# Kernel tuning notes

Measured on AMD Instinct MI355X. Metric: run time of the kernel, lower is better.

## Reference

```python
import jax, jax.numpy as jnp
import numpy as np

THETA = 10000.0

def _rope(x, cos, sin):
    # x: [B, S, D]; cos/sin: [S, D/2]. Pairs are (x[..., 2i], x[..., 2i+1]) treated as complex.
    xr = x.reshape(*x.shape[:-1], -1, 2)
    x0, x1 = xr[..., 0], xr[..., 1]
    o0 = x0 * cos - x1 * sin
    o1 = x0 * sin + x1 * cos
    return jnp.stack([o0, o1], axis=-1).reshape(x.shape)

def setup_inputs() -> dict:
    key = jax.random.key(0)
    ks = jax.random.split(key, 7)
    B, S, D = 4, 2048, 1024
    sd = 1.0 / np.sqrt(D)
    return {
        "x": jax.random.normal(ks[0], (B, S, D), dtype=jnp.float32),
        "wq_w": jax.random.normal(ks[1], (D, D), dtype=jnp.float32) * sd,
        "wq_b": jax.random.normal(ks[2], (D,), dtype=jnp.float32) * 0.01,
        "wk_w": jax.random.normal(ks[3], (D, D), dtype=jnp.float32) * sd,
        "wk_b": jax.random.normal(ks[4], (D,), dtype=jnp.float32) * 0.01,
        "wv_w": jax.random.normal(ks[5], (D, D), dtype=jnp.float32) * sd,
        "wv_b": jax.random.normal(ks[6], (D,), dtype=jnp.float32) * 0.01,
    }

def reference(x, wq_w, wq_b, wk_w, wk_b, wv_w, wv_b):
    B, S, D = x.shape
    # QKV projections (torch Linear: y = x @ W.T + b)
    q = jnp.einsum('bsd,ed->bse', x, wq_w) + wq_b
    k = jnp.einsum('bsd,ed->bse', x, wk_w) + wk_b
    v = jnp.einsum('bsd,ed->bse', x, wv_w) + wv_b
    # Rotary embedding: freqs_cis[t, i] = exp(i * t / theta^(2i/D))
    inv_freq = 1.0 / (THETA ** (jnp.arange(0, D, 2, dtype=jnp.float32) / D))  # [D/2]
    ang = jnp.arange(S, dtype=jnp.float32)[:, None] * inv_freq[None, :]  # [S, D/2]
    cos, sin = jnp.cos(ang), jnp.sin(ang)
    q = _rope(q, cos, sin)
    k = _rope(k, cos, sin)
    # Full (non-causal, single-head) attention with scale 1/sqrt(dim)
    scores = jnp.einsum('bqd,bkd->bqk', q, k) / jnp.sqrt(jnp.float32(D))
    probs = jax.nn.softmax(scores.astype(jnp.float32), axis=-1)
    return jnp.einsum('bqk,bkd->bqd', probs, v)
```

## Files before the change

### kernel.cpp

```cpp
#include <hip/hip_runtime.h>
#include <cstdint>

using u16 = unsigned short;
using u32 = unsigned int;

typedef __attribute__((ext_vector_type(8))) short short8;
typedef __attribute__((ext_vector_type(4))) float floatx4;

__device__ __forceinline__ u16 f2bf(float f) {
    u32 u = __float_as_uint(f);
    u32 r = u + 0x7fffu + ((u >> 16) & 1u);
    return (u16)(r >> 16);
}
__device__ __forceinline__ float bf2f(u16 h) {
    return __uint_as_float(((u32)h) << 16);
}

__global__ void cvt_f32_to_bf16(const float* __restrict__ in, u16* __restrict__ out, long n) {
    long i = ((long)blockIdx.x * blockDim.x + threadIdx.x) * 4;
    if (i >= n) return;
    float4 v = *reinterpret_cast<const float4*>(in + i);
    uint2 o;
    o.x = (u32)f2bf(v.x) | ((u32)f2bf(v.y) << 16);
    o.y = (u32)f2bf(v.z) | ((u32)f2bf(v.w) << 16);
    *reinterpret_cast<uint2*>(out + i) = o;
}

__global__ void cvt3(const float* __restrict__ w0, const float* __restrict__ w1,
                     const float* __restrict__ w2,
                     u16* __restrict__ o0, u16* __restrict__ o1, u16* __restrict__ o2,
                     const float* __restrict__ qb, const float* __restrict__ kb,
                     float* __restrict__ bqk) {
    int b = blockIdx.x;
    if (b >= 3072) {
        int i = (b - 3072) * 256 + threadIdx.x;
        bqk[i] = (i < 1024) ? qb[i] : kb[i - 1024];
        return;
    }
    int seg = b >> 10;
    const float* src; u16* dst;
    if (seg == 0)      { src = w0; dst = o0; }
    else if (seg == 1) { src = w1; dst = o1; }
    else               { src = w2; dst = o2; }
    long i = ((long)(b & 1023) * 256 + threadIdx.x) * 4;
    float4 v = *reinterpret_cast<const float4*>(src + i);
    uint2 o;
    o.x = (u32)f2bf(v.x) | ((u32)f2bf(v.y) << 16);
    o.y = (u32)f2bf(v.z) | ((u32)f2bf(v.w) << 16);
    *reinterpret_cast<uint2*>(dst + i) = o;
}

__device__ __forceinline__ void async_cp16(const u16* g, u16* l) {
    __builtin_amdgcn_global_load_lds(
        (const __attribute__((address_space(1))) void*)g,
        (__attribute__((address_space(3))) void*)l, 16, 0, 0);
}

template <bool BF16_OUT, bool ROPE>
__global__ __launch_bounds__(256)
void gemm_nt(const u16* __restrict__ A, const u16* __restrict__ B, void* __restrict__ Cv,
             int K, int lda, int ldb, int ldc,
             long sA, long sB, long sC,
             const float* __restrict__ bias_col, const float* __restrict__ bias_row,
             float scale)
{
    const u32 gx = gridDim.x, gy = gridDim.y;
    u32 id = blockIdx.x + gx * (blockIdx.y + gy * blockIdx.z);
    const u32 G = gx * gy * gridDim.z;
    if ((G & 7u) == 0u) {
        id = (id & 7u) * (G >> 3) + (id >> 3);
    }
    const u32 bx = id % gx;
    const u32 t1 = id / gx;
    const u32 by = t1 % gy;
    const u32 bz = t1 / gy;

    A += (long)bz * sA;
    B += (long)bz * sB;
    const long cbase = (long)bz * sC;

    __shared__ alignas(16) u16 smem[16384];
    u16* As = smem;
    u16* Bs = smem + 8192;

    const int tid  = threadIdx.x;
    const int lane = tid & 63;
    const int wave = tid >> 6;
    const int wm = (wave >> 1) << 6;
    const int wn = (wave & 1) << 6;

    const long tile_m = (long)by * 128;
    const long tile_n = (long)bx * 128;

    floatx4 acc[4][4] = {};

    const int srow = tid >> 2;
    const int skp  = (tid & 3) * 8;
    const u16* Ag = A + (tile_m + srow) * (long)lda + skp;
    const u16* Bg = B + (tile_n + srow) * (long)ldb + skp;
    u16* Asl = &As[tid * 8];
    u16* Bsl = &Bs[tid * 8];

    const int fm = lane & 15;
    const int fk = (lane >> 4) * 8;

    for (int k0 = 0; k0 < K; k0 += 64) {
        async_cp16(Ag,                       Asl);
        async_cp16(Ag + 64 * (long)lda,      Asl + 64 * 32);
        async_cp16(Ag + 32,                  Asl + 4096);
        async_cp16(Ag + 32 + 64 * (long)lda, Asl + 4096 + 64 * 32);
        async_cp16(Bg,                       Bsl);
        async_cp16(Bg + 64 * (long)ldb,      Bsl + 64 * 32);
        async_cp16(Bg + 32,                  Bsl + 4096);
        async_cp16(Bg + 32 + 64 * (long)ldb, Bsl + 4096 + 64 * 32);
        Ag += 64; Bg += 64;
        __syncthreads();

        #pragma unroll
        for (int c = 0; c < 2; ++c) {
            const u16* Ap = As + c * 4096;
            const u16* Bp = Bs + c * 4096;
            short8 af[4], bfr[4];
            #pragma unroll
            for (int i = 0; i < 4; ++i)
                af[i] = *reinterpret_cast<const short8*>(&Ap[(wm + i * 16 + fm) * 32 + fk]);
            #pragma unroll
            for (int j = 0; j < 4; ++j)
                bfr[j] = *reinterpret_cast<const short8*>(&Bp[(wn + j * 16 + fm) * 32 + fk]);
            #pragma unroll
            for (int i = 0; i < 4; ++i)
                #pragma unroll
                for (int j = 0; j < 4; ++j)
                    acc[i][j] = __builtin_amdgcn_mfma_f32_16x16x32_bf16(af[i], bfr[j], acc[i][j], 0, 0, 0);
        }
        __syncthreads();
    }

    const int q4  = lane >> 4;
    const int c16 = lane & 15;
    float* smemf  = (float*)smem;
    float* myeps = smemf + wave * (16 * 68);
    const long n0 = tile_n + wn + c16 * 4;

    float4 bc4 = make_float4(0.f, 0.f, 0.f, 0.f);
    if (bias_col) bc4 = *reinterpret_cast<const float4*>(bias_col + n0);

    float inv0 = 0.f, inv1 = 0.f;
    if constexpr (ROPE) {
        int p0 = (int)(n0 >> 1);
        inv0 = __expf((float)(p0 & 511)       * -1.79889463e-2f);
        inv1 = __expf((float)((p0 + 1) & 511) * -1.79889463e-2f);
    }

    #pragma unroll
    for (int i = 0; i < 4; ++i) {
        __syncthreads();
        #pragma unroll
        for (int j = 0; j < 4; ++j)
            #pragma unroll
            for (int r = 0; r < 4; ++r)
                myeps[(q4 * 4 + r) * 68 + j * 16 + c16] = acc[i][j][r];
        __syncthreads();
        #pragma unroll
        for (int p = 0; p < 4; ++p) {
            int lrow = p * 4 + q4;
            long m = tile_m + wm + i * 16 + lrow;
            float4 v = *reinterpret_cast<const float4*>(&myeps[lrow * 68 + c16 * 4]);
            v.x = v.x * scale + bc4.x;
            v.y = v.y * scale + bc4.y;
            v.z = v.z * scale + bc4.z;
            v.w = v.w * scale + bc4.w;
            if (bias_row) {
                float br = bias_row[m];
                v.x += br; v.y += br; v.z += br; v.w += br;
            }
            if constexpr (ROPE) {
                int s = (int)(m & 2047);
                float a0 = (float)s * inv0, a1 = (float)s * inv1;
                float sn0 = __sinf(a0), cs0 = __cosf(a0);
                float sn1 = __sinf(a1), cs1 = __cosf(a1);
                float x0 = v.x, x1 = v.y, x2 = v.z, x3 = v.w;
                v.x = x0 * cs0 - x1 * sn0;
                v.y = x0 * sn0 + x1 * cs0;
                v.z = x2 * cs1 - x3 * sn1;
                v.w = x2 * sn1 + x3 * cs1;
            }
            long off = cbase + m * (long)ldc + n0;
            if constexpr (BF16_OUT) {
                uint2 o;
                o.x = (u32)f2bf(v.x) | ((u32)f2bf(v.y) << 16);
                o.y = (u32)f2bf(v.z) | ((u32)f2bf(v.w) << 16);
                *reinterpret_cast<uint2*>((u16*)Cv + off) = o;
            } else {
                *reinterpret_cast<float4*>((float*)Cv + off) = v;
            }
        }
    }
}

__global__ __launch_bounds__(256)
void softmax_kernel(const u16* __restrict__ S, u16* __restrict__ P) {
    long row = blockIdx.x;
    const u16* s = S + row * 2048;
    u16* p = P + row * 2048;
    int tid = threadIdx.x;
    uint4 raw = *reinterpret_cast<const uint4*>(s + tid * 8);
    float v[8];
    v[0] = bf2f((u16)(raw.x & 0xffffu)); v[1] = bf2f((u16)(raw.x >> 16));
    v[2] = bf2f((u16)(raw.y & 0xffffu)); v[3] = bf2f((u16)(raw.y >> 16));
    v[4] = bf2f((u16)(raw.z & 0xffffu)); v[5] = bf2f((u16)(raw.z >> 16));
    v[6] = bf2f((u16)(raw.w & 0xffffu)); v[7] = bf2f((u16)(raw.w >> 16));
    float mx = v[0];
    #pragma unroll
    for (int j = 1; j < 8; ++j) mx = fmaxf(mx, v[j]);
    #pragma unroll
    for (int off = 32; off; off >>= 1) mx = fmaxf(mx, __shfl_xor(mx, off));
    __shared__ float redm[4];
    __shared__ float reds[4];
    int lane = tid & 63, wv = tid >> 6;
    if (lane == 0) redm[wv] = mx;
    __syncthreads();
    mx = fmaxf(fmaxf(redm[0], redm[1]), fmaxf(redm[2], redm[3]));
    float sum = 0.0f;
    #pragma unroll
    for (int j = 0; j < 8; ++j) { v[j] = __expf(v[j] - mx); sum += v[j]; }
    #pragma unroll
    for (int off = 32; off; off >>= 1) sum += __shfl_xor(sum, off);
    if (lane == 0) reds[wv] = sum;
    __syncthreads();
    sum = reds[0] + reds[1] + reds[2] + reds[3];
    float inv = 1.0f / sum;
    uint4 o;
    o.x = (u32)f2bf(v[0] * inv) | ((u32)f2bf(v[1] * inv) << 16);
    o.y = (u32)f2bf(v[2] * inv) | ((u32)f2bf(v[3] * inv) << 16);
    o.z = (u32)f2bf(v[4] * inv) | ((u32)f2bf(v[5] * inv) << 16);
    o.w = (u32)f2bf(v[6] * inv) | ((u32)f2bf(v[7] * inv) << 16);
    *reinterpret_cast<uint4*>(&p[tid * 8]) = o;
}

extern "C" void kernel_launch(void* const* d_in, const int* in_sizes, int n_in,
                              void* d_out, int out_size, void* d_ws, size_t ws_size,
                              hipStream_t stream)
{
    const float* x   = (const float*)d_in[0];
    const float* wqw = (const float*)d_in[1];
    const float* wqb = (const float*)d_in[2];
    const float* wkw = (const float*)d_in[3];
    const float* wkb = (const float*)d_in[4];
    const float* wvw = (const float*)d_in[5];
    const float* wvb = (const float*)d_in[6];
    float* out = (float*)d_out;

    char* ws = (char*)d_ws;
    const size_t MB = 1ull << 20;
    u16*   Sbuf = (u16*)(ws + 0);
    u16*   Pbuf = (u16*)(ws + 64 * MB);
    u16*   QK   = (u16*)(ws + 96 * MB);
    u16*   VT   = (u16*)(ws + 128 * MB);
    u16*   xb    = (u16*)(ws + 0);
    u16*   wqk   = (u16*)(ws + 16 * MB);
    u16*   wvbuf = (u16*)(ws + 20 * MB);
    float* bqk   = (float*)(ws + 22 * MB);

    cvt_f32_to_bf16<<<dim3(8192), 256, 0, stream>>>(x, xb, 8192L * 1024);
    cvt3<<<dim3(3080), 256, 0, stream>>>(wqw, wkw, wvw, wqk, wqk + 1024 * 1024, wvbuf,
                                         wqb, wkb, bqk);

    gemm_nt<true, true><<<dim3(16, 64, 1), 256, 0, stream>>>(
        xb, wqk, QK, 1024, 1024, 1024, 2048,
        0L, 0L, 0L, bqk, nullptr, 1.0f);

    gemm_nt<true, false><<<dim3(16, 8, 4), 256, 0, stream>>>(
        wvbuf, xb, VT, 1024, 1024, 1024, 2048,
        0L, 2048L * 1024, 1024L * 2048, nullptr, wvb, 1.0f);

    gemm_nt<true, false><<<dim3(16, 16, 4), 256, 0, stream>>>(
        QK, QK + 1024, Sbuf, 1024, 2048, 2048, 2048,
        2048L * 2048, 2048L * 2048, 2048L * 2048, nullptr, nullptr, 0.03125f);

    softmax_kernel<<<dim3(8192), 256, 0, stream>>>(Sbuf, Pbuf);

    gemm_nt<false, false><<<dim3(8, 16, 4), 256, 0, stream>>>(
        Pbuf, VT, out, 2048, 2048, 2048, 1024,
        2048L * 2048, 1024L * 2048, 2048L * 1024, nullptr, nullptr, 1.0f);

    (void)in_sizes; (void)n_in; (void)out_size; (void)ws_size;
}
```

Measured before the change: 280.5 us.

## Fuse QK and V projection GEMMs into one launch and swizzle LDS tiles

Merges the QK projection (with RoPE) and the transposed V projection into a single grid of 1536 blocks, so there is one launch and better tail utilization. It also XOR-swizzles the k-chunk position within LDS rows on both the async global-to-LDS copy and the fragment reads, to cut LDS bank conflicts in all GEMMs. RoPE becomes a runtime flag instead of a template parameter, which adds a uniform branch in the epilogue.

```diff
diff --git a/kernel.cpp b/kernel.cpp
--- a/kernel.cpp
+++ b/kernel.cpp
@@ -56,30 +56,14 @@
         (__attribute__((address_space(3))) void*)l, 16, 0, 0);
 }
 
-template <bool BF16_OUT, bool ROPE>
-__global__ __launch_bounds__(256)
-void gemm_nt(const u16* __restrict__ A, const u16* __restrict__ B, void* __restrict__ Cv,
-             int K, int lda, int ldb, int ldc,
-             long sA, long sB, long sC,
-             const float* __restrict__ bias_col, const float* __restrict__ bias_row,
-             float scale)
+template <bool BF16_OUT>
+__device__ __forceinline__ void gemm_core(
+    const u16* __restrict__ A, const u16* __restrict__ B, void* __restrict__ Cv,
+    int K, int lda, int ldb, int ldc,
+    long tile_m, long tile_n, long cbase,
+    const float* bias_col, const float* bias_row,
+    float scale, bool rope, u16* smem)
 {
-    const u32 gx = gridDim.x, gy = gridDim.y;
-    u32 id = blockIdx.x + gx * (blockIdx.y + gy * blockIdx.z);
-    const u32 G = gx * gy * gridDim.z;
-    if ((G & 7u) == 0u) {
-        id = (id & 7u) * (G >> 3) + (id >> 3);
-    }
-    const u32 bx = id % gx;
-    const u32 t1 = id / gx;
-    const u32 by = t1 % gy;
-    const u32 bz = t1 / gy;
-
-    A += (long)bz * sA;
-    B += (long)bz * sB;
-    const long cbase = (long)bz * sC;
-
-    __shared__ alignas(16) u16 smem[16384];
     u16* As = smem;
     u16* Bs = smem + 8192;
 
@@ -89,20 +73,17 @@
     const int wm = (wave >> 1) << 6;
     const int wn = (wave & 1) << 6;
 
-    const long tile_m = (long)by * 128;
-    const long tile_n = (long)bx * 128;
-
     floatx4 acc[4][4] = {};
 
     const int srow = tid >> 2;
-    const int skp  = (tid & 3) * 8;
+    const int skp  = (((tid & 3) ^ (srow & 3))) * 8;
     const u16* Ag = A + (tile_m + srow) * (long)lda + skp;
     const u16* Bg = B + (tile_n + srow) * (long)ldb + skp;
     u16* Asl = &As[tid * 8];
     u16* Bsl = &Bs[tid * 8];
 
-    const int fm = lane & 15;
-    const int fk = (lane >> 4) * 8;
+    const int fm  = lane & 15;
+    const int fks = (((lane >> 4) ^ (lane & 3))) * 8;
 
     for (int k0 = 0; k0 < K; k0 += 64) {
         async_cp16(Ag,                       Asl);
@@ -123,10 +104,10 @@
             short8 af[4], bfr[4];
             #pragma unroll
             for (int i = 0; i < 4; ++i)
-                af[i] = *reinterpret_cast<const short8*>(&Ap[(wm + i * 16 + fm) * 32 + fk]);
+                af[i] = *reinterpret_cast<const short8*>(&Ap[(wm + i * 16 + fm) * 32 + fks]);
             #pragma unroll
             for (int j = 0; j < 4; ++j)
-                bfr[j] = *reinterpret_cast<const short8*>(&Bp[(wn + j * 16 + fm) * 32 + fk]);
+                bfr[j] = *reinterpret_cast<const short8*>(&Bp[(wn + j * 16 + fm) * 32 + fks]);
             #pragma unroll
             for (int i = 0; i < 4; ++i)
                 #pragma unroll
@@ -146,7 +127,7 @@
     if (bias_col) bc4 = *reinterpret_cast<const float4*>(bias_col + n0);
 
     float inv0 = 0.f, inv1 = 0.f;
-    if constexpr (ROPE) {
+    if (rope) {
         int p0 = (int)(n0 >> 1);
         inv0 = __expf((float)(p0 & 511)       * -1.79889463e-2f);
         inv1 = __expf((float)((p0 + 1) & 511) * -1.79889463e-2f);
@@ -174,7 +155,7 @@
                 float br = bias_row[m];
                 v.x += br; v.y += br; v.z += br; v.w += br;
             }
-            if constexpr (ROPE) {
+            if (rope) {
                 int s = (int)(m & 2047);
                 float a0 = (float)s * inv0, a1 = (float)s * inv1;
                 float sn0 = __sinf(a0), cs0 = __cosf(a0);
@@ -198,6 +179,53 @@
     }
 }
 
+template <bool BF16_OUT>
+__global__ __launch_bounds__(256)
+void gemm_nt(const u16* __restrict__ A, const u16* __restrict__ B, void* __restrict__ Cv,
+             int K, int lda, int ldb, int ldc,
+             long sA, long sB, long sC,
+             const float* __restrict__ bias_col, const float* __restrict__ bias_row,
+             float scale)
+{
+    const u32 gx = gridDim.x, gy = gridDim.y;
+    u32 id = blockIdx.x + gx * (blockIdx.y + gy * blockIdx.z);
+    const u32 G = gx * gy * gridDim.z;
+    if ((G & 7u) == 0u) id = (id & 7u) * (G >> 3) + (id >> 3);
+    const u32 bx = id % gx;
+    const u32 t1 = id / gx;
+    const u32 by = t1 % gy;
+    const u32 bz = t1 / gy;
+
+    __shared__ alignas(16) u16 smem[16384];
+    gemm_core<BF16_OUT>(A + (long)bz * sA, B + (long)bz * sB, Cv,
+                        K, lda, ldb, ldc,
+                        (long)by * 128, (long)bx * 128, (long)bz * sC,
+                        bias_col, bias_row, scale, false, smem);
+}
+
+__global__ __launch_bounds__(256)
+void gemm_fused12(const u16* __restrict__ xb, const u16* __restrict__ wqk,
+                  const u16* __restrict__ wv, u16* __restrict__ QK, u16* __restrict__ VT,
+                  const float* __restrict__ bqk, const float* __restrict__ wvb)
+{
+    u32 id = blockIdx.x;
+    id = (id & 7u) * 192u + (id >> 3);
+    __shared__ alignas(16) u16 smem[16384];
+    if (id < 1024u) {
+        u32 bx = id & 15u, by = id >> 4;
+        gemm_core<true>(xb, wqk, QK, 1024, 1024, 1024, 2048,
+                        (long)by * 128, (long)bx * 128, 0L,
+                        bqk, nullptr, 1.0f, true, smem);
+    } else {
+        u32 r = id - 1024u;
+        u32 bx = r & 15u, by = (r >> 4) & 7u, bz = r >> 7;
+        gemm_core<true>(wv, xb + (long)bz * 2048 * 1024, VT,
+                        1024, 1024, 1024, 2048,
+                        (long)by * 128, (long)bx * 128, (long)bz * 1024 * 2048,
+                        nullptr, wvb, 1.0f, false, smem);
+    }
+}
+
 __global__ __launch_bounds__(256)
 void softmax_kernel(const u16* __restrict__ S, u16* __restrict__ P) {
     long row = blockIdx.x;
@@ -266,21 +294,15 @@
     cvt3<<<dim3(3080), 256, 0, stream>>>(wqw, wkw, wvw, wqk, wqk + 1024 * 1024, wvbuf,
                                          wqb, wkb, bqk);
 
-    gemm_nt<true, true><<<dim3(16, 64, 1), 256, 0, stream>>>(
-        xb, wqk, QK, 1024, 1024, 1024, 2048,
-        0L, 0L, 0L, bqk, nullptr, 1.0f);
-
-    gemm_nt<true, false><<<dim3(16, 8, 4), 256, 0, stream>>>(
-        wvbuf, xb, VT, 1024, 1024, 1024, 2048,
-        0L, 2048L * 1024, 1024L * 2048, nullptr, wvb, 1.0f);
-
-    gemm_nt<true, false><<<dim3(16, 16, 4), 256, 0, stream>>>(
+    gemm_fused12<<<dim3(1536), 256, 0, stream>>>(xb, wqk, wvbuf, QK, VT, bqk, wvb);
+
+    gemm_nt<true><<<dim3(16, 16, 4), 256, 0, stream>>>(
         QK, QK + 1024, Sbuf, 1024, 2048, 2048, 2048,
         2048L * 2048, 2048L * 2048, 2048L * 2048, nullptr, nullptr, 0.03125f);
 
     softmax_kernel<<<dim3(8192), 256, 0, stream>>>(Sbuf, Pbuf);
 
-    gemm_nt<false, false><<<dim3(8, 16, 4), 256, 0, stream>>>(
+    gemm_nt<false><<<dim3(8, 16, 4), 256, 0, stream>>>(
         Pbuf, VT, out, 2048, 2048, 2048, 1024,
         2048L * 2048, 1024L * 2048, 2048L * 1024, nullptr, nullptr, 1.0f);
 
```

Result: faster. 272.8 us (-2.8%).
